# Kernel optimization log

Hardware: AMD Instinct MI355X
Metric: run time of the kernel (lower is better)

The kernel has to match this reference:

```python
import jax, jax.numpy as jnp
import numpy as np

N_FEAT = 1024
NEG_BIG = -1e30  # finite stand-in for -inf to avoid NaNs on fully-masked rows


def setup_inputs() -> dict:
    key = jax.random.key(0)
    k1, k2, k3 = jax.random.split(key, 3)
    T, C = 4096, 1024
    x = jax.random.normal(k1, (T, C), dtype=jnp.float32)
    W = jax.random.normal(k2, (C, 3 * N_FEAT), dtype=jnp.float32) * 0.02
    b = jax.random.normal(k3, (3 * N_FEAT,), dtype=jnp.float32) * 0.02
    return {"x": x, "W": W, "b": b, "n_padd": 256}


def reference(x, W, b, n_padd):
    T, C = x.shape
    qkv = x @ W + b  # [T, 3*N_FEAT]
    q, k, v = jnp.split(qkv, 3, axis=1)  # each [T, N_FEAT]
    att = (q @ k.T) * (1.0 / jnp.sqrt(jnp.float32(N_FEAT)))  # [T, T]
    idx = jnp.arange(T)
    causal = idx[None, :] <= idx[:, None]
    data = (idx[None, :] >= n_padd) & (idx[:, None] >= n_padd)
    mask = causal & data
    att = jnp.where(mask, att, NEG_BIG)
    p = jax.nn.softmax(att, axis=-1)  # fully-masked rows -> uniform, zeroed below
    y = p @ v  # [T, N_FEAT]
    # kernel only stores rows >= n_padd; padded rows defined as zero here
    y = jnp.where(idx[:, None] >= n_padd, y, 0.0)
    return y
```

## Files before the change

kernel.cpp:

```cpp
#include <hip/hip_runtime.h>
#include <hip/hip_bf16.h>
#include <stdint.h>
#include <stddef.h>

#define TT 4096
#define CC 1024
#define NFD 1024
#define N3 3072
#define JSPLIT 17

typedef __bf16 bf16;
typedef __bf16 bf16x8 __attribute__((ext_vector_type(8)));
typedef __bf16 bf16x4 __attribute__((ext_vector_type(4)));
typedef float f32x4 __attribute__((ext_vector_type(4)));

typedef const __attribute__((address_space(1))) unsigned char gl_u8;
typedef __attribute__((address_space(3))) unsigned char lds_u8;

__device__ __forceinline__ void glds16(const void* g, void* l) {
  __builtin_amdgcn_global_load_lds((gl_u8*)g, (lds_u8*)l, 16, 0, 0);
}

__device__ __forceinline__ void stage128x32(const bf16* __restrict__ src, int ld, bf16* lds, int tid) {
  const int lane = tid & 63;
  const int w = tid >> 6;
#pragma unroll
  for (int p = 0; p < 2; ++p) {
    const int lbyte = w * 2048 + p * 1024;
    const int row = (lbyte >> 6) + (lane >> 2);
    const int kel = (lane & 3) << 3;
    glds16(src + row * ld + kel, (char*)lds + lbyte);
  }
}

__device__ __forceinline__ void gemm_core(const bf16* __restrict__ A, const bf16* __restrict__ B,
                                          int lda, int ldb, int ksteps,
                                          bf16* As, bf16* Bs, int tid, f32x4 (&acc)[4][4]) {
  const int lane = tid & 63;
  const int w = tid >> 6;
  const int wm = (w >> 1) * 64;
  const int wn = (w & 1) * 64;
  const int lrow = lane & 15;
  const int lko = (lane >> 4) * 8;
  stage128x32(A, lda, As, tid);
  stage128x32(B, ldb, Bs, tid);
  __syncthreads();
  for (int ks = 0; ks < ksteps; ++ks) {
    const bf16* Ac = As + (ks & 1) * 4096;
    const bf16* Bc = Bs + (ks & 1) * 4096;
    if (ks + 1 < ksteps) {
      stage128x32(A + (ks + 1) * 32, lda, As + ((ks + 1) & 1) * 4096, tid);
      stage128x32(B + (ks + 1) * 32, ldb, Bs + ((ks + 1) & 1) * 4096, tid);
    }
    bf16x8 af[4], bfr[4];
#pragma unroll
    for (int i = 0; i < 4; ++i)
      af[i] = *(const bf16x8*)(Ac + (wm + i * 16 + lrow) * 32 + lko);
#pragma unroll
    for (int i = 0; i < 4; ++i)
      bfr[i] = *(const bf16x8*)(Bc + (wn + i * 16 + lrow) * 32 + lko);
#pragma unroll
    for (int mi = 0; mi < 4; ++mi)
#pragma unroll
      for (int ni = 0; ni < 4; ++ni)
        acc[mi][ni] = __builtin_amdgcn_mfma_f32_16x16x32_bf16(af[mi], bfr[ni], acc[mi][ni], 0, 0, 0);
    __syncthreads();
  }
}

__global__ __launch_bounds__(256) void k_prep(const float* __restrict__ x, bf16* __restrict__ xb,
                                              const float* __restrict__ Wsrc, bf16* __restrict__ WbT) {
  __shared__ float Ls[64][68];
  const int tid = threadIdx.x;
  if (blockIdx.x < 2048) {
    int idx = (blockIdx.x * 256 + tid) * 8;
    f32x4 a = *(const f32x4*)(x + idx);
    f32x4 b = *(const f32x4*)(x + idx + 4);
    bf16x8 o;
#pragma unroll
    for (int j = 0; j < 4; ++j) { o[j] = (bf16)a[j]; o[4 + j] = (bf16)b[j]; }
    *(bf16x8*)(xb + idx) = o;
    return;
  }
  const int bid = blockIdx.x - 2048;
  const int n0 = (bid % 48) * 64;
  const int c0 = (bid / 48) * 64;
#pragma unroll
  for (int qq = 0; qq < 4; ++qq) {
    int lin = qq * 1024 + tid * 4;
    int r = lin >> 6, cc = lin & 63;
    f32x4 v = *(const f32x4*)(Wsrc + (size_t)(c0 + r) * N3 + n0 + cc);
#pragma unroll
    for (int j = 0; j < 4; ++j) Ls[r][cc + j] = v[j];
  }
  __syncthreads();
#pragma unroll
  for (int qq = 0; qq < 4; ++qq) {
    int lin = qq * 1024 + tid * 4;
    int nr = lin >> 6, cc = lin & 63;
    bf16x4 o;
#pragma unroll
    for (int j = 0; j < 4; ++j) o[j] = (bf16)Ls[cc + j][nr];
    *(bf16x4*)(WbT + (size_t)(n0 + nr) * CC + c0 + cc) = o;
  }
}

__global__ __launch_bounds__(256, 2) void k_qkv(const bf16* __restrict__ xb, const bf16* __restrict__ wbt,
                                                const float* __restrict__ bias,
                                                bf16* __restrict__ q, bf16* __restrict__ k,
                                                bf16* __restrict__ vT) {
  __shared__ bf16 As[2 * 128 * 32], Bs[2 * 128 * 32];
  const int tid = threadIdx.x;
  const int m0 = blockIdx.y * 128;
  const int n0 = blockIdx.x * 128;
  f32x4 acc[4][4];
#pragma unroll
  for (int i = 0; i < 4; ++i)
#pragma unroll
    for (int j = 0; j < 4; ++j) acc[i][j] = (f32x4){0.f, 0.f, 0.f, 0.f};

  gemm_core(xb + (size_t)m0 * CC, wbt + (size_t)n0 * CC, CC, CC, CC / 32, As, Bs, tid, acc);

  const int lane = tid & 63;
  const int w = tid >> 6;
  const int wm = (w >> 1) * 64, wn = (w & 1) * 64;
  const int seg = n0 >> 10;
#pragma unroll
  for (int mi = 0; mi < 4; ++mi) {
    const int tB = m0 + wm + mi * 16 + ((lane >> 4) << 2);
#pragma unroll
    for (int ni = 0; ni < 4; ++ni) {
      const int n = n0 + wn + ni * 16 + (lane & 15);
      const float bb = bias[n];
      f32x4 a = acc[mi][ni];
      if (seg == 2) {
        bf16x4 pv;
#pragma unroll
        for (int r = 0; r < 4; ++r) pv[r] = (bf16)(a[r] + bb);
        *(bf16x4*)(vT + (size_t)(n - 2048) * TT + tB) = pv;
      } else {
        bf16* dst = (seg == 0) ? q : k;
        const int nl = n & 1023;
#pragma unroll
        for (int r = 0; r < 4; ++r) dst[(size_t)(tB + r) * NFD + nl] = (bf16)(a[r] + bb);
      }
    }
  }
}

__global__ __launch_bounds__(256, 2) void k_scores(const bf16* __restrict__ q, const bf16* __restrict__ kk,
                                                   bf16* __restrict__ P, float* __restrict__ l,
                                                   const int* __restrict__ npadd_p) {
  const int id = blockIdx.x;
  const int lin = (id & 7) * 66 + (id >> 3);
  int band, rem;
  if (lin < 228)      { band = 0; rem = lin; }
  else if (lin < 392) { band = 1; rem = lin - 228; }
  else if (lin < 492) { band = 2; rem = lin - 392; }
  else                { band = 3; rem = lin - 492; }
  int it, jt;
  if (rem < 28) {
    int itp = (int)((sqrtf(8.0f * (float)rem + 1.0f) - 1.0f) * 0.5f);
    while ((itp + 1) * (itp + 2) / 2 <= rem) ++itp;
    while (itp * (itp + 1) / 2 > rem) --itp;
    it = band * 8 + itp;
    jt = band * 8 + (rem - itp * (itp + 1) / 2);
  } else {
    const int rem2 = rem - 28;
    it = band * 8 + 7 + (rem2 >> 3);
    jt = band * 8 + (rem2 & 7);
  }
  const int np = *npadd_p;
  const int jt0 = np >> 7;
  if (jt < jt0) return;

  __shared__ bf16 As[2 * 128 * 32], Bs[2 * 128 * 32];
  const int tid = threadIdx.x;
  f32x4 acc[4][4];
#pragma unroll
  for (int i = 0; i < 4; ++i)
#pragma unroll
    for (int j = 0; j < 4; ++j) acc[i][j] = (f32x4){0.f, 0.f, 0.f, 0.f};

  gemm_core(q + (size_t)it * 128 * CC, kk + (size_t)jt * 128 * CC, CC, CC, CC / 32, As, Bs, tid, acc);

  const int lane = tid & 63;
  const int w = tid >> 6;
  const int wm = (w >> 1) * 64, wn = (w & 1) * 64;
  const float scale = 0.03125f;
#pragma unroll
  for (int mi = 0; mi < 4; ++mi) {
    const int iB = it * 128 + wm + mi * 16 + ((lane >> 4) << 2);
    float rs[4] = {0.f, 0.f, 0.f, 0.f};
#pragma unroll
    for (int ni = 0; ni < 4; ++ni) {
      const int j = jt * 128 + wn + ni * 16 + (lane & 15);
      f32x4 a = acc[mi][ni];
#pragma unroll
      for (int r = 0; r < 4; ++r) {
        const int i = iB + r;
        float p = 0.f;
        if (j <= i && j >= np && i >= np) p = __expf(a[r] * scale);
        const bf16 pb = (bf16)p;
        P[(size_t)i * TT + j] = pb;
        rs[r] += (float)pb;
      }
    }
#pragma unroll
    for (int r = 0; r < 4; ++r) {
      float v = rs[r];
      v += __shfl_xor(v, 1);
      v += __shfl_xor(v, 2);
      v += __shfl_xor(v, 4);
      v += __shfl_xor(v, 8);
      if ((lane & 15) == 0) atomicAdd(&l[iB + r], v);
    }
  }
}

__global__ __launch_bounds__(256, 2) void k_pvc(const bf16* __restrict__ P, const bf16* __restrict__ vT,
                                                bf16* __restrict__ part0, bf16* __restrict__ part1,
                                                const float* __restrict__ l, float* __restrict__ y,
                                                const int* __restrict__ npadd_p) {
  const int c = blockIdx.x;
  const int it = blockIdx.y;
  const int d0 = blockIdx.z * 128;
  const int np = *npadd_p;
  const int jt0 = np >> 7;
  int jlo, jhi;
  if (c == 0) { jlo = jt0;              jhi = min(JSPLIT, it + 1); }
  else        { jlo = max(JSPLIT, jt0); jhi = it + 1; }
  if (jlo >= jhi) return;

  __shared__ bf16 As[2 * 128 * 32], Bs[2 * 128 * 32];
  const int tid = threadIdx.x;
  f32x4 acc[4][4];
#pragma unroll
  for (int i = 0; i < 4; ++i)
#pragma unroll
    for (int j = 0; j < 4; ++j) acc[i][j] = (f32x4){0.f, 0.f, 0.f, 0.f};

  gemm_core(P + (size_t)it * 128 * TT + (size_t)jlo * 128,
            vT + (size_t)d0 * TT + (size_t)jlo * 128,
            TT, TT, (jhi - jlo) * 4, As, Bs, tid, acc);

  const int lane = tid & 63;
  const int w = tid >> 6;
  const int wm = (w >> 1) * 64, wn = (w & 1) * 64;
  const bool sole = (c == 0) ? (jhi == it + 1) : (jlo == jt0);
  if (sole) {
#pragma unroll
    for (int mi = 0; mi < 4; ++mi) {
      const int iB = it * 128 + wm + mi * 16 + ((lane >> 4) << 2);
      float inv4[4];
#pragma unroll
      for (int r = 0; r < 4; ++r) {
        const int i = iB + r;
        inv4[r] = (i >= np) ? (1.0f / l[i]) : 0.0f;
      }
#pragma unroll
      for (int ni = 0; ni < 4; ++ni) {
        const int d = d0 + wn + ni * 16 + (lane & 15);
        f32x4 a = acc[mi][ni];
#pragma unroll
        for (int r = 0; r < 4; ++r)
          y[(size_t)(iB + r) * NFD + d] = a[r] * inv4[r];
      }
    }
  } else {
    bf16* __restrict__ part = (c == 0) ? part0 : part1;
#pragma unroll
    for (int mi = 0; mi < 4; ++mi) {
      const int iB = it * 128 + wm + mi * 16 + ((lane >> 4) << 2);
#pragma unroll
      for (int ni = 0; ni < 4; ++ni) {
        const int d = d0 + wn + ni * 16 + (lane & 15);
        f32x4 a = acc[mi][ni];
#pragma unroll
        for (int r = 0; r < 4; ++r)
          part[(size_t)(iB + r) * NFD + d] = (bf16)a[r];
      }
    }
  }
}

__global__ __launch_bounds__(256) void k_norm(const bf16* __restrict__ part0, const bf16* __restrict__ part1,
                                              const float* __restrict__ l, float* __restrict__ y,
                                              const int* __restrict__ npadd_p) {
  const int idx = (blockIdx.x * 256 + threadIdx.x) * 8;
  const int i = idx >> 10;
  const int np = *npadd_p;
  const int jt0 = np >> 7;
  const int it = i >> 7;
  if (i < np) {
    f32x4 z = (f32x4){0.f, 0.f, 0.f, 0.f};
    *(f32x4*)(y + idx) = z;
    *(f32x4*)(y + idx + 4) = z;
    return;
  }
  if ((it + 1 <= JSPLIT) || (jt0 >= JSPLIT)) return;
  const float inv = 1.0f / l[i];
  bf16x8 a = *(const bf16x8*)(part0 + idx);
  bf16x8 b = *(const bf16x8*)(part1 + idx);
  f32x4 o0, o1;
#pragma unroll
  for (int j = 0; j < 4; ++j) {
    o0[j] = ((float)a[j] + (float)b[j]) * inv;
    o1[j] = ((float)a[4 + j] + (float)b[4 + j]) * inv;
  }
  *(f32x4*)(y + idx) = o0;
  *(f32x4*)(y + idx + 4) = o1;
}

extern "C" void kernel_launch(void* const* d_in, const int* in_sizes, int n_in,
                              void* d_out, int out_size, void* d_ws, size_t ws_size,
                              hipStream_t stream) {
  const float* x = (const float*)d_in[0];
  const float* W = (const float*)d_in[1];
  const float* b = (const float*)d_in[2];
  const int* npadd = (const int*)d_in[3];
  float* y = (float*)d_out;

  char* ws = (char*)d_ws;
  const size_t MB = 1u << 20;
  bf16* q  = (bf16*)(ws + 0 * MB);
  bf16* kk = (bf16*)(ws + 8 * MB);
  bf16* part0 = (bf16*)(ws + 0 * MB);
  bf16* part1 = (bf16*)(ws + 8 * MB);
  bf16* vT = (bf16*)(ws + 16 * MB);
  float* l = (float*)(ws + 24 * MB);
  bf16* P  = (bf16*)(ws + 24 * MB + 65536);
  bf16* xb = P;
  bf16* WbT = (bf16*)((char*)P + 8 * MB);

  k_prep<<<dim3(2048 + 768), 256, 0, stream>>>(x, xb, W, WbT);
  k_qkv<<<dim3(N3 / 128, TT / 128), 256, 0, stream>>>(xb, WbT, b, q, kk, vT);
  hipMemsetAsync(l, 0, TT * sizeof(float), stream);
  k_scores<<<dim3(528), 256, 0, stream>>>(q, kk, P, l, npadd);
  k_pvc<<<dim3(2, TT / 128, NFD / 128), 256, 0, stream>>>(P, vT, part0, part1, l, y, npadd);
  k_norm<<<dim3((TT * NFD) / (256 * 8)), 256, 0, stream>>>(part0, part1, l, y, npadd);
}
```

Baseline: 128.5 us.

## Split PV split-K reduction into four key-range chunks with compact partial buffers

The P@V kernel now splits the causal key range into four chunks (0-9, 9-17, 17-25, 25-32 tiles) instead of two. This shortens the longest per-block K loop and adds more blocks for load balance. Partials from chunks 0-2 go to offset-compacted bf16 buffers that fit the workspace. Chunk 3 writes unnormalized fp32 into y, and the norm kernel sums whichever chunks are active before dividing by l. The cost is extra partial-buffer traffic and a more complex reduction step.

```diff
diff --git a/kernel.cpp b/kernel.cpp
--- a/kernel.cpp
+++ b/kernel.cpp
@@ -7,7 +7,8 @@
 #define CC 1024
 #define NFD 1024
 #define N3 3072
-#define JSPLIT 17
+#define PB0 1152
+#define PB2 2176
 
 typedef __bf16 bf16;
 typedef __bf16 bf16x8 __attribute__((ext_vector_type(8)));
@@ -220,6 +221,7 @@
 
 __global__ __launch_bounds__(256, 2) void k_pvc(const bf16* __restrict__ P, const bf16* __restrict__ vT,
                                                 bf16* __restrict__ part0, bf16* __restrict__ part1,
+                                                bf16* __restrict__ part2,
                                                 const float* __restrict__ l, float* __restrict__ y,
                                                 const int* __restrict__ npadd_p) {
   const int c = blockIdx.x;
@@ -227,9 +229,10 @@
   const int d0 = blockIdx.z * 128;
   const int np = *npadd_p;
   const int jt0 = np >> 7;
-  int jlo, jhi;
-  if (c == 0) { jlo = jt0;              jhi = min(JSPLIT, it + 1); }
-  else        { jlo = max(JSPLIT, jt0); jhi = it + 1; }
+  const int lo = (c == 0) ? 0 : (c == 1 ? 9 : (c == 2 ? 17 : 25));
+  const int hi = (c == 0) ? 9 : (c == 1 ? 17 : (c == 2 ? 25 : 32));
+  const int jlo = max(lo, jt0);
+  const int jhi = min(hi, it + 1);
   if (jlo >= jhi) return;
 
   __shared__ bf16 As[2 * 128 * 32], Bs[2 * 128 * 32];
@@ -247,7 +250,7 @@
   const int lane = tid & 63;
   const int w = tid >> 6;
   const int wm = (w >> 1) * 64, wn = (w & 1) * 64;
-  const bool sole = (c == 0) ? (jhi == it + 1) : (jlo == jt0);
+  const bool sole = (jlo == jt0) && (jhi == it + 1);
   if (sole) {
 #pragma unroll
     for (int mi = 0; mi < 4; ++mi) {
@@ -267,8 +270,7 @@
           y[(size_t)(iB + r) * NFD + d] = a[r] * inv4[r];
       }
     }
-  } else {
-    bf16* __restrict__ part = (c == 0) ? part0 : part1;
+  } else if (c == 3) {
 #pragma unroll
     for (int mi = 0; mi < 4; ++mi) {
       const int iB = it * 128 + wm + mi * 16 + ((lane >> 4) << 2);
@@ -278,36 +280,75 @@
         f32x4 a = acc[mi][ni];
 #pragma unroll
         for (int r = 0; r < 4; ++r)
-          part[(size_t)(iB + r) * NFD + d] = (bf16)a[r];
+          y[(size_t)(iB + r) * NFD + d] = a[r];
+      }
+    }
+  } else {
+    bf16* __restrict__ part = (c == 0) ? part0 : (c == 1 ? part1 : part2);
+    const int base = (c == 2) ? (PB2 * NFD) : (PB0 * NFD);
+#pragma unroll
+    for (int mi = 0; mi < 4; ++mi) {
+      const int iB = it * 128 + wm + mi * 16 + ((lane >> 4) << 2);
+#pragma unroll
+      for (int ni = 0; ni < 4; ++ni) {
+        const int d = d0 + wn + ni * 16 + (lane & 15);
+        f32x4 a = acc[mi][ni];
+#pragma unroll
+        for (int r = 0; r < 4; ++r)
+          part[(size_t)(iB + r) * NFD + d - base] = (bf16)a[r];
       }
     }
   }
 }
 
 __global__ __launch_bounds__(256) void k_norm(const bf16* __restrict__ part0, const bf16* __restrict__ part1,
+                                              const bf16* __restrict__ part2,
                                               const float* __restrict__ l, float* __restrict__ y,
                                               const int* __restrict__ npadd_p) {
   const int idx = (blockIdx.x * 256 + threadIdx.x) * 8;
   const int i = idx >> 10;
   const int np = *npadd_p;
-  const int jt0 = np >> 7;
-  const int it = i >> 7;
   if (i < np) {
     f32x4 z = (f32x4){0.f, 0.f, 0.f, 0.f};
     *(f32x4*)(y + idx) = z;
     *(f32x4*)(y + idx + 4) = z;
     return;
   }
-  if ((it + 1 <= JSPLIT) || (jt0 >= JSPLIT)) return;
+  const int jt0 = np >> 7;
+  const int it = i >> 7;
+  const int ip1 = it + 1;
+  const bool a0 = (max(0, jt0)  < min(9, ip1));
+  const bool a1 = (max(9, jt0)  < min(17, ip1));
+  const bool a2 = (max(17, jt0) < min(25, ip1));
+  const bool a3 = (max(25, jt0) < min(32, ip1));
+  const int cnt = (int)a0 + (int)a1 + (int)a2 + (int)a3;
+  if (cnt <= 1) return;
+  float s[8] = {0.f, 0.f, 0.f, 0.f, 0.f, 0.f, 0.f, 0.f};
+  if (a0) {
+    bf16x8 a = *(const bf16x8*)(part0 + idx - PB0 * NFD);
+#pragma unroll
+    for (int j = 0; j < 8; ++j) s[j] += (float)a[j];
+  }
+  if (a1) {
+    bf16x8 a = *(const bf16x8*)(part1 + idx - PB0 * NFD);
+#pragma unroll
+    for (int j = 0; j < 8; ++j) s[j] += (float)a[j];
+  }
+  if (a2) {
+    bf16x8 a = *(const bf16x8*)(part2 + idx - PB2 * NFD);
+#pragma unroll
+    for (int j = 0; j < 8; ++j) s[j] += (float)a[j];
+  }
+  if (a3) {
+    f32x4 a = *(const f32x4*)(y + idx);
+    f32x4 b = *(const f32x4*)(y + idx + 4);
+#pragma unroll
+    for (int j = 0; j < 4; ++j) { s[j] += a[j]; s[4 + j] += b[j]; }
+  }
   const float inv = 1.0f / l[i];
-  bf16x8 a = *(const bf16x8*)(part0 + idx);
-  bf16x8 b = *(const bf16x8*)(part1 + idx);
   f32x4 o0, o1;
 #pragma unroll
-  for (int j = 0; j < 4; ++j) {
-    o0[j] = ((float)a[j] + (float)b[j]) * inv;
-    o1[j] = ((float)a[4 + j] + (float)b[4 + j]) * inv;
-  }
+  for (int j = 0; j < 4; ++j) { o0[j] = s[j] * inv; o1[j] = s[4 + j] * inv; }
   *(f32x4*)(y + idx) = o0;
   *(f32x4*)(y + idx + 4) = o1;
 }
@@ -326,7 +367,8 @@
   bf16* q  = (bf16*)(ws + 0 * MB);
   bf16* kk = (bf16*)(ws + 8 * MB);
   bf16* part0 = (bf16*)(ws + 0 * MB);
-  bf16* part1 = (bf16*)(ws + 8 * MB);
+  bf16* part1 = (bf16*)(ws + (size_t)(TT - PB0) * NFD * 2);
+  bf16* part2 = (bf16*)(ws + (size_t)2 * (TT - PB0) * NFD * 2);
   bf16* vT = (bf16*)(ws + 16 * MB);
   float* l = (float*)(ws + 24 * MB);
   bf16* P  = (bf16*)(ws + 24 * MB + 65536);
@@ -337,6 +379,6 @@
   k_qkv<<<dim3(N3 / 128, TT / 128), 256, 0, stream>>>(xb, WbT, b, q, kk, vT);
   hipMemsetAsync(l, 0, TT * sizeof(float), stream);
   k_scores<<<dim3(528), 256, 0, stream>>>(q, kk, P, l, npadd);
-  k_pvc<<<dim3(2, TT / 128, NFD / 128), 256, 0, stream>>>(P, vT, part0, part1, l, y, npadd);
-  k_norm<<<dim3((TT * NFD) / (256 * 8)), 256, 0, stream>>>(part0, part1, l, y, npadd);
-}
+  k_pvc<<<dim3(4, TT / 128, NFD / 128), 256, 0, stream>>>(P, vT, part0, part1, part2, l, y, npadd);
+  k_norm<<<dim3((TT * NFD) / (256 * 8)), 256, 0, stream>>>(part0, part1, part2, l, y, npadd);
+}
```

Result: faster. 125.1 us (-2.6%).
